# Performance work log

Hardware: AMD Instinct MI355X
Metric: run time of the kernel (lower is better)

Reference implementation:

```python
import jax, jax.numpy as jnp
import numpy as np
from functools import partial

C = 10   # number of regular-repr fields
G = 4    # C4 rotation group order
EPS = 1e-5


def _lift_kernel(w):
    """Lifting (trivial->regular) P4 kernel. w: [C, Cin, k, k] ->
    full kernel [C*G, Cin, k, k] with output channel layout (field, orientation)."""
    ks = [jnp.rot90(w, r, axes=(-2, -1)) for r in range(G)]  # each [C,Cin,k,k]
    k = jnp.stack(ks, axis=1)                                 # [C,G,Cin,k,k]
    return k.reshape(w.shape[0] * G, w.shape[1], w.shape[2], w.shape[3])


def _gconv_kernel(w):
    """Regular->regular P4 kernel. w: [Cout, Cin, G, k, k] (indexed by relative
    input orientation) -> full kernel [Cout*G, Cin*G, k, k].
    K[co*G+r, ci*G+s] = rot90(w[co, ci, (s-r) mod G], r)."""
    Cout, Cin, _, k1, k2 = w.shape
    ks = []
    for r in range(G):
        wr = jnp.roll(w, shift=r, axis=2)             # wr[..., s, :, :] = w[..., (s-r)%G]
        wr = jnp.rot90(wr, r, axes=(-2, -1))          # rotate spatially by r*90deg
        ks.append(wr)
    k = jnp.stack(ks, axis=1)                          # [Cout, G, Cin, G, k, k]
    return k.reshape(Cout * G, Cin * G, k1, k2)


def _conv(x, k, pad):
    return jax.lax.conv_general_dilated(
        x, k, window_strides=(1, 1), padding=pad,
        dimension_numbers=('NCHW', 'OIHW', 'NCHW'))


def _bn_relu(x, gamma, beta):
    """InnerBatchNorm (stats shared over the G orientations of each field) + ReLU."""
    B, CG, H, W = x.shape
    xr = x.reshape(B, C, G, H, W)
    m = xr.mean(axis=(0, 2, 3, 4), keepdims=True)
    v = xr.var(axis=(0, 2, 3, 4), keepdims=True)
    g = gamma[None, :, None, None, None]
    b = beta[None, :, None, None, None]
    y = (xr - m) * jax.lax.rsqrt(v + EPS) * g + b
    return jnp.maximum(y.reshape(B, CG, H, W), 0.0)


def _maxpool2(x):
    return jax.lax.reduce_window(x, -jnp.inf, jax.lax.max,
                                 (1, 1, 2, 2), (1, 1, 2, 2), 'VALID')


def setup_inputs() -> dict:
    key = jax.random.key(0)
    ks = jax.random.split(key, 20)
    B = 1024
    x = jax.random.normal(ks[0], (B, 1, 28, 28), dtype=jnp.float32)
    w1 = jax.random.normal(ks[1], (C, 1, 3, 3), dtype=jnp.float32) * 0.3
    w2 = jax.random.normal(ks[2], (C, C, G, 3, 3), dtype=jnp.float32) * 0.1
    w3 = jax.random.normal(ks[3], (C, C, G, 3, 3), dtype=jnp.float32) * 0.1
    w4 = jax.random.normal(ks[4], (C, C, G, 3, 3), dtype=jnp.float32) * 0.1
    w5 = jax.random.normal(ks[5], (C, C, G, 3, 3), dtype=jnp.float32) * 0.1
    w6 = jax.random.normal(ks[6], (C, C, G, 3, 3), dtype=jnp.float32) * 0.1
    w7 = jax.random.normal(ks[7], (C, C, G, 4, 4), dtype=jnp.float32) * 0.1
    g1 = jnp.ones((C,), jnp.float32) + 0.1 * jax.random.normal(ks[8], (C,))
    b1 = 0.1 * jax.random.normal(ks[9], (C,))
    g2 = jnp.ones((C,), jnp.float32) + 0.1 * jax.random.normal(ks[10], (C,))
    b2 = 0.1 * jax.random.normal(ks[11], (C,))
    gs = jnp.ones((C,), jnp.float32) + 0.1 * jax.random.normal(ks[12], (C,))
    bs = 0.1 * jax.random.normal(ks[13], (C,))
    wfc = jax.random.normal(ks[14], (10, C * 11 * 11), dtype=jnp.float32) * 0.05
    bfc = jnp.zeros((10,), jnp.float32)
    return dict(x=x, w1=w1, w2=w2, w3=w3, w4=w4, w5=w5, w6=w6, w7=w7,
                g1=g1, b1=b1, g2=g2, b2=b2, gs=gs, bs=bs, wfc=wfc, bfc=bfc)


PAD1 = [(1, 1), (1, 1)]
PAD0 = [(0, 0), (0, 0)]


def reference(x, w1, w2, w3, w4, w5, w6, w7, g1, b1, g2, b2, gs, bs, wfc, bfc):
    # block1: lifting P4 conv 3x3 pad1 + InnerBN + ReLU  -> [B, 40, 28, 28]
    h = _bn_relu(_conv(x, _lift_kernel(w1), PAD1), g1, b1)
    # block2: P4 conv + BN + ReLU + 2x2 max pool         -> [B, 40, 14, 14]
    h = _maxpool2(_bn_relu(_conv(h, _gconv_kernel(w2), PAD1), g2, b2))
    # blocks 3-6: P4 conv + shared BN/ReLU               -> [B, 40, 14, 14]
    for w in (w3, w4, w5, w6):
        h = _bn_relu(_conv(h, _gconv_kernel(w), PAD1), gs, bs)
    # block7: P4 conv 4x4 pad0 + shared BN/ReLU          -> [B, 40, 11, 11]
    h = _bn_relu(_conv(h, _gconv_kernel(w7), PAD0), gs, bs)
    # group pooling: max over the G orientations of each field -> [B, 10, 11, 11]
    B = h.shape[0]
    h = h.reshape(B, C, G, 11, 11).max(axis=2)
    # fc
    return h.reshape(B, -1) @ wfc.T + bfc
```

## Files before the change

kernel.cpp:

```cpp
#include <hip/hip_runtime.h>

#define EPSV 1e-5f
#define INV28 (1.f / 3211264.f)
#define INV14 (1.f / 802816.f)
#define INV11 (1.f / 495616.f)
#define NCOPY 64
#define LSTRIDE 2048

typedef _Float16 v8h __attribute__((ext_vector_type(8)));
typedef _Float16 v4h __attribute__((ext_vector_type(4)));
typedef _Float16 v2h __attribute__((ext_vector_type(2)));
typedef float v4f __attribute__((ext_vector_type(4)));

__device__ __forceinline__ int h2i(v2h v) { union { v2h h; int i; } u; u.h = v; return u.i; }
__device__ __forceinline__ v2h i2h(int i) { union { v2h h; int i; } u; u.i = i; return u.h; }
__device__ __forceinline__ int pmax2(int a, int b) {
  v2h x = i2h(a), y = i2h(b), r;
  r[0] = x[0] > y[0] ? x[0] : y[0];
  r[1] = x[1] > y[1] ? x[1] : y[1];
  return h2i(r);
}

__device__ __forceinline__ int rotsrc(int r, int dy, int dx, int K) {
  int sy, sx;
  if (r == 0)      { sy = dy;       sx = dx; }
  else if (r == 1) { sy = dx;       sx = K - 1 - dy; }
  else if (r == 2) { sy = K - 1 - dy; sx = K - 1 - dx; }
  else             { sy = K - 1 - dx; sx = dy; }
  return sy * K + sx;
}

__device__ __forceinline__ float gw_val(const float* __restrict__ w, int oc, int g,
                                        int j, int KS) {
  int tap = g / 5, cig = g % 5, ci = cig * 8 + j;
  int co = oc >> 2, r = oc & 3, cin = ci >> 2, s = ci & 3;
  int srel = (s - r) & 3;
  return w[((co * 10 + cin) * 4 + srel) * (KS * KS) + rotsrc(r, tap / KS, tap % KS, KS)];
}

__device__ __forceinline__ float statN(const float* __restrict__ p, int i) {
  float v = 0.f;
#pragma unroll
  for (int c = 0; c < NCOPY; ++c) v += p[c * 32 + i];
  return v;
}

__global__ void prep_kernel(const float* __restrict__ w1, const float* __restrict__ w2,
                            const float* __restrict__ w3, const float* __restrict__ w4,
                            const float* __restrict__ w5, const float* __restrict__ w6,
                            const float* __restrict__ w7,
                            _Float16* __restrict__ K1h, _Float16* __restrict__ Wh,
                            float* __restrict__ stats) {
  int idx = blockIdx.x * blockDim.x + threadIdx.x;
  if (idx < 7 * LSTRIDE) { stats[idx] = 0.f; return; }
  idx -= 7 * LSTRIDE;
  if (idx < 1536) {
    int mt = idx >> 9, l = (idx >> 3) & 63, j = idx & 7;
    int m = l & 15, quad = l >> 4;
    int k = quad * 8 + j, oc = mt * 16 + m;
    float val = 0.f;
    if (k < 9 && oc < 40) {
      int c = oc >> 2, r = oc & 3;
      val = w1[c * 9 + rotsrc(r, k / 3, k % 3, 3)];
    }
    K1h[idx] = (_Float16)val;
    return;
  }
  idx -= 1536;
  if (idx < 92160) {
    int l = idx / 18432, r0 = idx % 18432;
    const float* w = (l == 0) ? w2 : (l == 1) ? w3 : (l == 2) ? w4 : (l == 3) ? w5 : w6;
    int mt = r0 / 6144, r1 = r0 % 6144;
    int c = r1 / 512, r2 = r1 % 512;
    int q = r2 / 128, r3 = r2 % 128;
    int ocl = r3 / 8, j = r3 % 8;
    int oc = mt * 16 + ocl, g = c * 4 + q;
    float val = 0.f;
    if (oc < 40 && g < 45) val = gw_val(w, oc, g, j, 3);
    Wh[idx] = (_Float16)val;
    return;
  }
  idx -= 92160;
  if (idx < 30720) {
    int mt = idx / 10240, r1 = idx % 10240;
    int c = r1 / 512, r2 = r1 % 512;
    int q = r2 / 128, r3 = r2 % 128;
    int ocl = r3 / 8, j = r3 % 8;
    int oc = mt * 16 + ocl, g = c * 4 + q;
    float val = 0.f;
    if (oc < 40) val = gw_val(w7, oc, g, j, 4);
    Wh[92160 + idx] = (_Float16)val;
  }
}

__global__ __launch_bounds__(256) void conv1_stats(
    const float* __restrict__ x, const _Float16* __restrict__ K1h,
    float* __restrict__ stats) {
  __shared__ float ximg[900];
  __shared__ float sstat[20];
  const int tid = threadIdx.x, img = blockIdx.x;
  if (tid < 20) sstat[tid] = 0.f;
  for (int i = tid; i < 900; i += 256) {
    int gy = i / 30 - 1, gx = i % 30 - 1;
    ximg[i] = (gy >= 0 && gy < 28 && gx >= 0 && gx < 28)
                  ? x[img * 784 + gy * 28 + gx] : 0.f;
  }
  __syncthreads();
  const int lane = tid & 63, wv = tid >> 6;
  const int m = lane & 15, quad = lane >> 4;
  v8h a1[3];
#pragma unroll
  for (int mt = 0; mt < 3; ++mt)
    a1[mt] = *(const v8h*)(K1h + (mt * 64 + lane) * 8);
  float s[3] = {0.f, 0.f, 0.f}, q[3] = {0.f, 0.f, 0.f};
  for (int st = wv; st < 49; st += 4) {
    const int p = st * 16 + m;
    const int y = p / 28, xx = p % 28;
    v8h b;
#pragma unroll
    for (int j = 0; j < 8; ++j) {
      const int t = quad * 8 + j;
      float v = 0.f;
      if (t < 9) v = ximg[(y + t / 3) * 30 + xx + t % 3];
      b[j] = (_Float16)v;
    }
#pragma unroll
    for (int mt = 0; mt < 3; ++mt) {
      v4f acc = {0.f, 0.f, 0.f, 0.f};
      acc = __builtin_amdgcn_mfma_f32_16x16x32_f16(a1[mt], b, acc, 0, 0, 0);
#pragma unroll
      for (int r = 0; r < 4; ++r) { float v = acc[r]; s[mt] += v; q[mt] += v * v; }
    }
  }
#pragma unroll
  for (int mt = 0; mt < 3; ++mt) {
    float sv = s[mt], qv = q[mt];
#pragma unroll
    for (int off = 1; off <= 8; off <<= 1) {
      sv += __shfl_xor(sv, off, 64);
      qv += __shfl_xor(qv, off, 64);
    }
    if (m == 0 && ((mt < 2) || (quad < 2))) {
      atomicAdd(&sstat[mt * 4 + quad], sv);
      atomicAdd(&sstat[10 + mt * 4 + quad], qv);
    }
  }
  __syncthreads();
  if (tid < 20) atomicAdd(&stats[(blockIdx.x & (NCOPY - 1)) * 32 + tid], sstat[tid]);
}

template<int R>
__device__ __forceinline__ void band_impl(
    const int img, const int y0,
    const float* __restrict__ x, const _Float16* __restrict__ K1h,
    const _Float16* __restrict__ Wl,
    float* __restrict__ xpatch, _Float16* __restrict__ tile,
    const float* __restrict__ sc, const float* __restrict__ sh,
    float* __restrict__ sstat, _Float16* __restrict__ T0) {
  constexpr int NPIX = R * 28, NSUB = NPIX / 16, NSW = (NSUB + 3) / 4;
  constexpr int SROWS = R + 2, XR = R + 4;
  const int tid = threadIdx.x;
  const int lane = tid & 63, wv = tid >> 6;
  const int m = lane & 15, quad = lane >> 4;

  for (int i = tid; i < XR * 32; i += 256) {
    int gy = y0 - 2 + i / 32, gx = i % 32 - 2;
    xpatch[i] = (gy >= 0 && gy < 28 && gx >= 0 && gx < 28)
                    ? x[(long)img * 784 + gy * 28 + gx] : 0.f;
  }
  __syncthreads();

  {
    v8h a1[3];
#pragma unroll
    for (int mt = 0; mt < 3; ++mt)
      a1[mt] = *(const v8h*)(K1h + (mt * 64 + lane) * 8);
    constexpr int NPIXS = SROWS * 30;
    constexpr int NST = (NPIXS + 15) / 16;
    for (int st = wv; st < NST; st += 4) {
      const int p = st * 16 + m;
      const int pc = p < NPIXS ? p : NPIXS - 1;
      const int iy = pc / 30, ix = pc % 30;
      v8h b;
#pragma unroll
      for (int j = 0; j < 8; ++j) {
        const int t = quad * 8 + j;
        float v = 0.f;
        if (t < 9) v = xpatch[(iy + t / 3) * 32 + ix + t % 3];
        b[j] = (_Float16)v;
      }
      const int gy = y0 + iy - 1, gx = ix - 1;
      const bool wr = p < NPIXS;
      const bool inb = wr && gy >= 0 && gy < 28 && gx >= 0 && gx < 28;
      _Float16* tb = &tile[pc * 40];
#pragma unroll
      for (int mt = 0; mt < 3; ++mt) {
        v4f a = {0.f, 0.f, 0.f, 0.f};
        a = __builtin_amdgcn_mfma_f32_16x16x32_f16(a1[mt], b, a, 0, 0, 0);
        if (((mt < 2) || (quad < 2)) && wr) {
          const int f = mt * 4 + quad;
          const float scf = sc[f], shf = sh[f];
          v4h pk;
#pragma unroll
          for (int r = 0; r < 4; ++r)
            pk[r] = inb ? (_Float16)fmaxf(0.f, fmaf(a[r], scf, shf)) : (_Float16)0.f;
          *(v4h*)(tb + mt * 16 + quad * 4) = pk;
        }
      }
    }
  }
  __syncthreads();

  int pbase[NSW];
  bool sv[NSW];
#pragma unroll
  for (int s = 0; s < NSW; ++s) {
    int ns = wv + 4 * s;
    sv[s] = ns < NSUB;
    int i = (sv[s] ? ns : 0) * 16 + m;
    int q = i >> 2, c2 = i & 3;
    int yy = 2 * (q / 14) + (c2 >> 1), xx = 2 * (q % 14) + (c2 & 1);
    pbase[s] = (yy * 30 + xx) * 40;
  }
  v4f acc[3][NSW] = {};

  const _Float16* wlane = Wl + (quad * 16 + m) * 8;
  for (int c = 0; c < 12; ++c) {
    int g = 4 * c + quad; g = g > 44 ? 44 : g;
    int tap = g / 5, cig = g - tap * 5;
    int boff = ((tap / 3) * 30 + (tap % 3)) * 40 + cig * 8;
    v8h bfr[NSW];
#pragma unroll
    for (int s = 0; s < NSW; ++s)
      if (sv[s]) bfr[s] = *(const v8h*)&tile[pbase[s] + boff];
    v8h afr[3];
#pragma unroll
    for (int mt = 0; mt < 3; ++mt)
      afr[mt] = *(const v8h*)(wlane + (mt * 12 + c) * 512);
#pragma unroll
    for (int s = 0; s < NSW; ++s)
      if (sv[s]) {
#pragma unroll
        for (int mt = 0; mt < 3; ++mt)
          acc[mt][s] = __builtin_amdgcn_mfma_f32_16x16x32_f16(afr[mt], bfr[s],
                                                             acc[mt][s], 0, 0, 0);
      }
  }

#pragma unroll
  for (int mt = 0; mt < 3; ++mt) {
    float svv = 0.f, qvv = 0.f;
#pragma unroll
    for (int s = 0; s < NSW; ++s)
      if (sv[s]) {
#pragma unroll
        for (int r = 0; r < 4; ++r) { float v = acc[mt][s][r]; svv += v; qvv += v * v; }
      }
    const bool ocok = (mt < 2) || (quad < 2);
#pragma unroll
    for (int off = 1; off <= 8; off <<= 1) {
      svv += __shfl_xor(svv, off, 64);
      qvv += __shfl_xor(qvv, off, 64);
    }
    if (m == 0 && ocok) {
      atomicAdd(&sstat[mt * 4 + quad], svv);
      atomicAdd(&sstat[10 + mt * 4 + quad], qvv);
    }
  }

#pragma unroll
  for (int s = 0; s < NSW; ++s) {
    if (!sv[s]) continue;
    const int ns = wv + 4 * s;
    const int q = ns * 4 + (m >> 2);
    const int tb4 = (img * 256 + (y0 / 2 + q / 14 + 1) * 16 + (q % 14 + 1)) * 40;
#pragma unroll
    for (int mt = 0; mt < 3; ++mt) {
      const bool ocok = (mt < 2) || (quad < 2);
      if (!ocok) continue;
      v2h w0, w1;
      w0[0] = (_Float16)acc[mt][s][0]; w0[1] = (_Float16)acc[mt][s][1];
      w1[0] = (_Float16)acc[mt][s][2]; w1[1] = (_Float16)acc[mt][s][3];
      int a0 = h2i(w0), a1 = h2i(w1);
      a0 = pmax2(a0, __shfl_xor(a0, 1, 64));
      a0 = pmax2(a0, __shfl_xor(a0, 2, 64));
      a1 = pmax2(a1, __shfl_xor(a1, 1, 64));
      a1 = pmax2(a1, __shfl_xor(a1, 2, 64));
      if ((m & 3) == 0) {
        v2h r0 = i2h(a0), r1 = i2h(a1);
        v4h o;
        o[0] = r0[0]; o[1] = r0[1]; o[2] = r1[0]; o[3] = r1[1];
        *(v4h*)(T0 + (long)tb4 + mt * 16 + quad * 4) = o;
      }
    }
  }
}

__global__ __launch_bounds__(256) void conv_band_all(
    const float* __restrict__ x, const _Float16* __restrict__ K1h,
    const _Float16* __restrict__ Wl, const float* __restrict__ pstats,
    const float* __restrict__ pgamma, const float* __restrict__ pbeta,
    _Float16* __restrict__ T0, float* __restrict__ stats) {
  __shared__ __attribute__((aligned(16))) _Float16 tile[6 * 30 * 40];
  __shared__ float xpatch[8 * 32];
  __shared__ float sc[10], sh[10], sstat[20];
  const int tid = threadIdx.x;
  if (tid < 20) sstat[tid] = 0.f;
  if (tid >= 32 && tid < 42) {
    int f = tid - 32;
    float mu = statN(pstats, f) * INV28, q = statN(pstats, 10 + f) * INV28;
    float isd = rsqrtf(q - mu * mu + EPSV);
    float s = pgamma[f] * isd;
    sc[f] = s; sh[f] = pbeta[f] - mu * s;
  }
  const int bid = blockIdx.x;
  const int img = bid / 7, y0 = (bid % 7) * 4;
  band_impl<4>(img, y0, x, K1h, Wl, xpatch, tile, sc, sh, sstat, T0);
  __syncthreads();
  if (tid < 20) atomicAdd(&stats[(bid & (NCOPY - 1)) * 32 + tid], sstat[tid]);
}

__global__ __launch_bounds__(256) void conv_tile(
    _Float16* T, const _Float16* __restrict__ Wl,
    const float* __restrict__ pstats, const float* __restrict__ pg,
    const float* __restrict__ pb, float pinvn, float* __restrict__ stG) {
  __shared__ __attribute__((aligned(16))) _Float16 tile[256 * 40];
  __shared__ v2h scH[10], shH[10];
  __shared__ float sstat[20];
  const int tid = threadIdx.x, img = blockIdx.x;
  const int lane = tid & 63, wv = tid >> 6;
  const int m = lane & 15, quad = lane >> 4;
  if (tid < 20) sstat[tid] = 0.f;
  if (tid >= 32 && tid < 42) {
    int f = tid - 32;
    float mu = statN(pstats, f) * pinvn, q = statN(pstats, 10 + f) * pinvn;
    float isd = rsqrtf(q - mu * mu + EPSV);
    float s = pg[f] * isd;
    _Float16 sH = (_Float16)s, hH = (_Float16)(pb[f] - mu * s);
    v2h t0, t1;
    t0[0] = sH; t0[1] = sH; t1[0] = hH; t1[1] = hH;
    scH[f] = t0; shH[f] = t1;
  }
  __syncthreads();
  {
    const int iy = tid >> 4, ix = tid & 15;
    const bool border = (iy == 0) | (iy == 15) | (ix == 0) | (ix == 15);
    const _Float16* src = T + ((long)img * 256 + tid) * 40;
    _Float16* dst = &tile[tid * 40];
    if (!border) {
#pragma unroll
      for (int cg5 = 0; cg5 < 5; ++cg5) {
        v8h rv = *(const v8h*)(src + cg5 * 8);
        v2h* r2 = (v2h*)&rv;
        v8h pk; v2h* p2 = (v2h*)&pk;
#pragma unroll
        for (int pr = 0; pr < 4; ++pr) {
          const int f = cg5 * 2 + (pr >> 1);
          v2h t = r2[pr] * scH[f] + shH[f];
          v2h o;
          o[0] = t[0] > (_Float16)0.f ? t[0] : (_Float16)0.f;
          o[1] = t[1] > (_Float16)0.f ? t[1] : (_Float16)0.f;
          p2[pr] = o;
        }
        *(v8h*)(dst + cg5 * 8) = pk;
      }
    } else {
      v8h z;
#pragma unroll
      for (int u = 0; u < 8; ++u) z[u] = (_Float16)0.f;
#pragma unroll
      for (int cg5 = 0; cg5 < 5; ++cg5) *(v8h*)(dst + cg5 * 8) = z;
    }
  }
  __syncthreads();

  int pb3[4], n3[4];
  bool sv3[4], va3[4];
#pragma unroll
  for (int s = 0; s < 4; ++s) {
    int ns = wv + 4 * s;
    sv3[s] = ns < 13;
    int n = ns * 16 + m;
    va3[s] = sv3[s] && (n < 196);
    n = n < 196 ? n : 195;
    n3[s] = n;
    pb3[s] = ((n / 14) * 16 + (n % 14)) * 40;
  }
  const int wofs = (quad * 16 + m) * 8;
  v4f acc[3][4];
#pragma unroll
  for (int mt = 0; mt < 3; ++mt)
#pragma unroll
    for (int s = 0; s < 4; ++s) acc[mt][s] = (v4f){0.f, 0.f, 0.f, 0.f};
  for (int c = 0; c < 12; ++c) {
    int g = 4 * c + quad; g = g > 44 ? 44 : g;
    int tap = g / 5, cig = g - tap * 5;
    int boff = ((tap / 3) * 16 + (tap % 3)) * 40 + cig * 8;
    v8h bfr[4];
#pragma unroll
    for (int s = 0; s < 4; ++s)
      if (sv3[s]) bfr[s] = *(const v8h*)&tile[pb3[s] + boff];
    v8h afr[3];
#pragma unroll
    for (int mt = 0; mt < 3; ++mt)
      afr[mt] = *(const v8h*)(Wl + wofs + (mt * 12 + c) * 512);
#pragma unroll
    for (int s = 0; s < 4; ++s)
      if (sv3[s]) {
#pragma unroll
        for (int mt = 0; mt < 3; ++mt)
          acc[mt][s] = __builtin_amdgcn_mfma_f32_16x16x32_f16(afr[mt], bfr[s],
                                                             acc[mt][s], 0, 0, 0);
      }
  }

#pragma unroll
  for (int mt = 0; mt < 3; ++mt) {
    float svv = 0.f, qvv = 0.f;
#pragma unroll
    for (int s = 0; s < 4; ++s)
      if (va3[s]) {
#pragma unroll
        for (int r = 0; r < 4; ++r) { float v = acc[mt][s][r]; svv += v; qvv += v * v; }
      }
    const bool ocok = (mt < 2) || (quad < 2);
#pragma unroll
    for (int off = 1; off <= 8; off <<= 1) {
      svv += __shfl_xor(svv, off, 64);
      qvv += __shfl_xor(qvv, off, 64);
    }
    if (m == 0 && ocok) {
      atomicAdd(&sstat[mt * 4 + quad], svv);
      atomicAdd(&sstat[10 + mt * 4 + quad], qvv);
    }
  }
  __syncthreads();
  if (tid < 20) atomicAdd(&stG[(blockIdx.x & (NCOPY - 1)) * 32 + tid], sstat[tid]);

#pragma unroll
  for (int mt = 0; mt < 3; ++mt) {
    const bool ocok = (mt < 2) || (quad < 2);
    if (!ocok) continue;
#pragma unroll
    for (int s = 0; s < 4; ++s)
      if (va3[s]) {
        v4h pk;
#pragma unroll
        for (int r = 0; r < 4; ++r) pk[r] = (_Float16)acc[mt][s][r];
        const int n = n3[s];
        *(v4h*)(T + ((long)img * 256 + (n / 14 + 1) * 16 + (n % 14 + 1)) * 40
                + mt * 16 + quad * 4) = pk;
      }
  }
}

__global__ __launch_bounds__(256) void conv7_tile(
    const _Float16* __restrict__ Tin, const _Float16* __restrict__ Wl,
    const float* __restrict__ pstats, const float* __restrict__ pg,
    const float* __restrict__ pb,
    _Float16* __restrict__ T7, float* __restrict__ stG) {
  __shared__ __attribute__((aligned(16))) _Float16 tile[256 * 40];
  __shared__ v2h scH[10], shH[10];
  __shared__ float sstat[20];
  const int tid = threadIdx.x, img = blockIdx.x;
  const int lane = tid & 63, wv = tid >> 6;
  const int m = lane & 15, quad = lane >> 4;
  if (tid < 20) sstat[tid] = 0.f;
  if (tid >= 32 && tid < 42) {
    int f = tid - 32;
    float mu = statN(pstats, f) * INV14, q = statN(pstats, 10 + f) * INV14;
    float isd = rsqrtf(q - mu * mu + EPSV);
    float s = pg[f] * isd;
    _Float16 sH = (_Float16)s, hH = (_Float16)(pb[f] - mu * s);
    v2h t0, t1;
    t0[0] = sH; t0[1] = sH; t1[0] = hH; t1[1] = hH;
    scH[f] = t0; shH[f] = t1;
  }
  __syncthreads();
  {
    const int iy = tid >> 4, ix = tid & 15;
    const bool border = (iy == 0) | (iy == 15) | (ix == 0) | (ix == 15);
    const _Float16* src = Tin + ((long)img * 256 + tid) * 40;
    _Float16* dst = &tile[tid * 40];
    if (!border) {
#pragma unroll
      for (int cg5 = 0; cg5 < 5; ++cg5) {
        v8h rv = *(const v8h*)(src + cg5 * 8);
        v2h* r2 = (v2h*)&rv;
        v8h pk; v2h* p2 = (v2h*)&pk;
#pragma unroll
        for (int pr = 0; pr < 4; ++pr) {
          const int f = cg5 * 2 + (pr >> 1);
          v2h t = r2[pr] * scH[f] + shH[f];
          v2h o;
          o[0] = t[0] > (_Float16)0.f ? t[0] : (_Float16)0.f;
          o[1] = t[1] > (_Float16)0.f ? t[1] : (_Float16)0.f;
          p2[pr] = o;
        }
        *(v8h*)(dst + cg5 * 8) = pk;
      }
    } else {
      v8h z;
#pragma unroll
      for (int u = 0; u < 8; ++u) z[u] = (_Float16)0.f;
#pragma unroll
      for (int cg5 = 0; cg5 < 5; ++cg5) *(v8h*)(dst + cg5 * 8) = z;
    }
  }
  __syncthreads();

  int pb7[2], n7[2];
  bool va7[2];
#pragma unroll
  for (int s = 0; s < 2; ++s) {
    int ns = wv + 4 * s;
    int n = ns * 16 + m;
    va7[s] = n < 121;
    n = n < 121 ? n : 120;
    n7[s] = n;
    pb7[s] = ((n / 11 + 1) * 16 + (n % 11 + 1)) * 40;
  }
  const int wofs = (quad * 16 + m) * 8;
  v4f acc[3][2];
#pragma unroll
  for (int mt = 0; mt < 3; ++mt)
#pragma unroll
    for (int s = 0; s < 2; ++s) acc[mt][s] = (v4f){0.f, 0.f, 0.f, 0.f};
  for (int c = 0; c < 20; ++c) {
    int g = 4 * c + quad;
    int tap = g / 5, cig = g - tap * 5;
    int boff = ((tap >> 2) * 16 + (tap & 3)) * 40 + cig * 8;
    v8h bfr[2];
#pragma unroll
    for (int s = 0; s < 2; ++s) bfr[s] = *(const v8h*)&tile[pb7[s] + boff];
    v8h afr[3];
#pragma unroll
    for (int mt = 0; mt < 3; ++mt)
      afr[mt] = *(const v8h*)(Wl + wofs + (mt * 20 + c) * 512);
#pragma unroll
    for (int s = 0; s < 2; ++s)
#pragma unroll
      for (int mt = 0; mt < 3; ++mt)
        acc[mt][s] = __builtin_amdgcn_mfma_f32_16x16x32_f16(afr[mt], bfr[s],
                                                           acc[mt][s], 0, 0, 0);
  }

#pragma unroll
  for (int mt = 0; mt < 3; ++mt) {
    float svv = 0.f, qvv = 0.f;
#pragma unroll
    for (int s = 0; s < 2; ++s)
      if (va7[s]) {
#pragma unroll
        for (int r = 0; r < 4; ++r) { float v = acc[mt][s][r]; svv += v; qvv += v * v; }
      }
    const bool ocok = (mt < 2) || (quad < 2);
#pragma unroll
    for (int off = 1; off <= 8; off <<= 1) {
      svv += __shfl_xor(svv, off, 64);
      qvv += __shfl_xor(qvv, off, 64);
    }
    if (m == 0 && ocok) {
      atomicAdd(&sstat[mt * 4 + quad], svv);
      atomicAdd(&sstat[10 + mt * 4 + quad], qvv);
    }
  }
  __syncthreads();
  if (tid < 20) atomicAdd(&stG[(blockIdx.x & (NCOPY - 1)) * 32 + tid], sstat[tid]);

#pragma unroll
  for (int mt = 0; mt < 3; ++mt) {
    const bool ocok = (mt < 2) || (quad < 2);
    if (!ocok) continue;
#pragma unroll
    for (int s = 0; s < 2; ++s)
      if (va7[s]) {
        v4h pk;
#pragma unroll
        for (int r = 0; r < 4; ++r) pk[r] = (_Float16)acc[mt][s][r];
        *(v4h*)(T7 + ((long)img * 121 + n7[s]) * 40 + mt * 16 + quad * 4) = pk;
      }
  }
}

__global__ __launch_bounds__(256) void head_kernel(
    const _Float16* __restrict__ T7, const float* __restrict__ stats7,
    const float* __restrict__ gs, const float* __restrict__ bs,
    const float* __restrict__ wfc, const float* __restrict__ bfc,
    float* __restrict__ out) {
  __shared__ float sc[10], sh[10];
  __shared__ float mbuf[1210];
  __shared__ float red[40];
  const int tid = threadIdx.x, img = blockIdx.x;
  if (tid < 10) {
    float mu = statN(stats7, tid) * INV11, q = statN(stats7, 10 + tid) * INV11;
    float isd = rsqrtf(q - mu * mu + EPSV);
    float s = gs[tid] * isd;
    sc[tid] = s;
    sh[tid] = bs[tid] - mu * s;
  }
  __syncthreads();
  for (int p = tid; p < 121; p += 256) {
    const _Float16* rp = T7 + ((long)img * 121 + p) * 40;
#pragma unroll
    for (int cg5 = 0; cg5 < 5; ++cg5) {
      v8h v = *(const v8h*)(rp + cg5 * 8);
#pragma unroll
      for (int fh = 0; fh < 2; ++fh) {
        const int f = cg5 * 2 + fh;
        float mx = fmaf((float)v[fh * 4], sc[f], sh[f]);
#pragma unroll
        for (int r = 1; r < 4; ++r)
          mx = fmaxf(mx, fmaf((float)v[fh * 4 + r], sc[f], sh[f]));
        mbuf[f * 121 + p] = fmaxf(0.f, mx);
      }
    }
  }
  __syncthreads();
  const int wv = tid >> 6;
  for (int k = 0; k < 10; ++k) {
    float p = 0.f;
    for (int j = tid; j < 1210; j += 256) p = fmaf(mbuf[j], wfc[k * 1210 + j], p);
#pragma unroll
    for (int off = 32; off > 0; off >>= 1) p += __shfl_xor(p, off, 64);
    if ((tid & 63) == 0) red[k * 4 + wv] = p;
  }
  __syncthreads();
  if (tid < 10)
    out[img * 10 + tid] = bfc[tid] + red[tid * 4] + red[tid * 4 + 1] +
                          red[tid * 4 + 2] + red[tid * 4 + 3];
}

extern "C" void kernel_launch(void* const* d_in, const int* in_sizes, int n_in,
                              void* d_out, int out_size, void* d_ws, size_t ws_size,
                              hipStream_t stream) {
  const float* x   = (const float*)d_in[0];
  const float* w1  = (const float*)d_in[1];
  const float* w2  = (const float*)d_in[2];
  const float* w3  = (const float*)d_in[3];
  const float* w4  = (const float*)d_in[4];
  const float* w5  = (const float*)d_in[5];
  const float* w6  = (const float*)d_in[6];
  const float* w7  = (const float*)d_in[7];
  const float* g1  = (const float*)d_in[8];
  const float* b1  = (const float*)d_in[9];
  const float* g2  = (const float*)d_in[10];
  const float* b2  = (const float*)d_in[11];
  const float* gs  = (const float*)d_in[12];
  const float* bs  = (const float*)d_in[13];
  const float* wfc = (const float*)d_in[14];
  const float* bfc = (const float*)d_in[15];

  float* ws = (float*)d_ws;
  float* stats  = ws;
  _Float16* K1h = (_Float16*)(ws + 14336);
  _Float16* Wh  = (_Float16*)(ws + 15104);
  _Float16* T0  = (_Float16*)(ws + 76544);
  _Float16* T7  = (_Float16*)(ws + 5319424L);

  prep_kernel<<<543, 256, 0, stream>>>(w1, w2, w3, w4, w5, w6, w7, K1h, Wh, stats);
  conv1_stats<<<1024, 256, 0, stream>>>(x, K1h, stats);
  conv_band_all<<<7168, 256, 0, stream>>>(x, K1h, Wh, stats, g1, b1, T0,
                                          stats + LSTRIDE);
  conv_tile<<<1024, 256, 0, stream>>>(T0, Wh + 18432, stats + LSTRIDE, g2, b2, INV28,
                                      stats + 2 * LSTRIDE);
  conv_tile<<<1024, 256, 0, stream>>>(T0, Wh + 36864, stats + 2 * LSTRIDE, gs, bs, INV14,
                                      stats + 3 * LSTRIDE);
  conv_tile<<<1024, 256, 0, stream>>>(T0, Wh + 55296, stats + 3 * LSTRIDE, gs, bs, INV14,
                                      stats + 4 * LSTRIDE);
  conv_tile<<<1024, 256, 0, stream>>>(T0, Wh + 73728, stats + 4 * LSTRIDE, gs, bs, INV14,
                                      stats + 5 * LSTRIDE);
  conv7_tile<<<1024, 256, 0, stream>>>(T0, Wh + 92160, stats + 5 * LSTRIDE, gs, bs,
                                       T7, stats + 6 * LSTRIDE);
  head_kernel<<<1024, 256, 0, stream>>>(T7, stats + 6 * LSTRIDE, gs, bs, wfc, bfc,
                                        (float*)d_out);
}
```

Measured before the change: 311.6 us.

## Merge weight prep into conv1 stats kernel and shrink stat replica count

Folds the weight-packing prep kernel into the conv1 statistics kernel: the first 486 blocks pack the weights, and the remaining 1024 blocks compute per-image stats, building the lifting kernel fragments directly from w1 in registers. Stats zeroing moves to hipMemsetAsync. NCOPY drops from 64 to 8, so each stats read sums fewer replicas, at the cost of more atomic contention on each copy. This removes one kernel launch and the dependency between prep and conv1, but adds a memset node and redundant per-lane w1 gathers.

```diff
diff --git a/kernel.cpp b/kernel.cpp
--- a/kernel.cpp
+++ b/kernel.cpp
@@ -4,8 +4,8 @@
 #define INV28 (1.f / 3211264.f)
 #define INV14 (1.f / 802816.f)
 #define INV11 (1.f / 495616.f)
-#define NCOPY 64
-#define LSTRIDE 2048
+#define NCOPY 8
+#define LSTRIDE 256
 
 typedef _Float16 v8h __attribute__((ext_vector_type(8)));
 typedef _Float16 v4h __attribute__((ext_vector_type(4)));
@@ -38,6 +38,18 @@
   return w[((co * 10 + cin) * 4 + srel) * (KS * KS) + rotsrc(r, tap / KS, tap % KS, KS)];
 }
 
+__device__ __forceinline__ _Float16 k1_val(const float* __restrict__ w1,
+                                           int lane, int mt, int j) {
+  const int m = lane & 15, quad = lane >> 4;
+  const int k = quad * 8 + j, oc = mt * 16 + m;
+  float val = 0.f;
+  if (k < 9 && oc < 40) {
+    int c = oc >> 2, r = oc & 3;
+    val = w1[c * 9 + rotsrc(r, k / 3, k % 3, 3)];
+  }
+  return (_Float16)val;
+}
+
 __device__ __forceinline__ float statN(const float* __restrict__ p, int i) {
   float v = 0.f;
 #pragma unroll
@@ -45,60 +57,54 @@
   return v;
 }
 
-__global__ void prep_kernel(const float* __restrict__ w1, const float* __restrict__ w2,
-                            const float* __restrict__ w3, const float* __restrict__ w4,
-                            const float* __restrict__ w5, const float* __restrict__ w6,
-                            const float* __restrict__ w7,
-                            _Float16* __restrict__ K1h, _Float16* __restrict__ Wh,
-                            float* __restrict__ stats) {
-  int idx = blockIdx.x * blockDim.x + threadIdx.x;
-  if (idx < 7 * LSTRIDE) { stats[idx] = 0.f; return; }
-  idx -= 7 * LSTRIDE;
-  if (idx < 1536) {
-    int mt = idx >> 9, l = (idx >> 3) & 63, j = idx & 7;
-    int m = l & 15, quad = l >> 4;
-    int k = quad * 8 + j, oc = mt * 16 + m;
-    float val = 0.f;
-    if (k < 9 && oc < 40) {
-      int c = oc >> 2, r = oc & 3;
-      val = w1[c * 9 + rotsrc(r, k / 3, k % 3, 3)];
-    }
-    K1h[idx] = (_Float16)val;
-    return;
-  }
-  idx -= 1536;
-  if (idx < 92160) {
-    int l = idx / 18432, r0 = idx % 18432;
-    const float* w = (l == 0) ? w2 : (l == 1) ? w3 : (l == 2) ? w4 : (l == 3) ? w5 : w6;
-    int mt = r0 / 6144, r1 = r0 % 6144;
-    int c = r1 / 512, r2 = r1 % 512;
-    int q = r2 / 128, r3 = r2 % 128;
-    int ocl = r3 / 8, j = r3 % 8;
-    int oc = mt * 16 + ocl, g = c * 4 + q;
-    float val = 0.f;
-    if (oc < 40 && g < 45) val = gw_val(w, oc, g, j, 3);
-    Wh[idx] = (_Float16)val;
-    return;
-  }
-  idx -= 92160;
-  if (idx < 30720) {
-    int mt = idx / 10240, r1 = idx % 10240;
-    int c = r1 / 512, r2 = r1 % 512;
-    int q = r2 / 128, r3 = r2 % 128;
-    int ocl = r3 / 8, j = r3 % 8;
-    int oc = mt * 16 + ocl, g = c * 4 + q;
-    float val = 0.f;
-    if (oc < 40) val = gw_val(w7, oc, g, j, 4);
-    Wh[92160 + idx] = (_Float16)val;
-  }
-}
-
-__global__ __launch_bounds__(256) void conv1_stats(
-    const float* __restrict__ x, const _Float16* __restrict__ K1h,
+__global__ __launch_bounds__(256) void prep_stats(
+    const float* __restrict__ x,
+    const float* __restrict__ w1, const float* __restrict__ w2,
+    const float* __restrict__ w3, const float* __restrict__ w4,
+    const float* __restrict__ w5, const float* __restrict__ w6,
+    const float* __restrict__ w7,
+    _Float16* __restrict__ K1h, _Float16* __restrict__ Wh,
     float* __restrict__ stats) {
   __shared__ float ximg[900];
   __shared__ float sstat[20];
-  const int tid = threadIdx.x, img = blockIdx.x;
+  const int tid = threadIdx.x;
+  if (blockIdx.x < 486) {
+    int idx = blockIdx.x * blockDim.x + tid;
+    if (idx < 1536) {
+      int mt = idx >> 9, l = (idx >> 3) & 63, j = idx & 7;
+      K1h[idx] = k1_val(w1, l, mt, j);
+      return;
+    }
+    idx -= 1536;
+    if (idx < 92160) {
+      int l = idx / 18432, r0 = idx % 18432;
+      const float* w = (l == 0) ? w2 : (l == 1) ? w3 : (l == 2) ? w4
+                                                : (l == 3) ? w5 : w6;
+      int mt = r0 / 6144, r1 = r0 % 6144;
+      int c = r1 / 512, r2 = r1 % 512;
+      int q = r2 / 128, r3 = r2 % 128;
+      int ocl = r3 / 8, j = r3 % 8;
+      int oc = mt * 16 + ocl, g = c * 4 + q;
+      float val = 0.f;
+      if (oc < 40 && g < 45) val = gw_val(w, oc, g, j, 3);
+      Wh[idx] = (_Float16)val;
+      return;
+    }
+    idx -= 92160;
+    {
+      int mt = idx / 10240, r1 = idx % 10240;
+      int c = r1 / 512, r2 = r1 % 512;
+      int q = r2 / 128, r3 = r2 % 128;
+      int ocl = r3 / 8, j = r3 % 8;
+      int oc = mt * 16 + ocl, g = c * 4 + q;
+      float val = 0.f;
+      if (oc < 40) val = gw_val(w7, oc, g, j, 4);
+      Wh[92160 + idx] = (_Float16)val;
+    }
+    return;
+  }
+
+  const int img = blockIdx.x - 486;
   if (tid < 20) sstat[tid] = 0.f;
   for (int i = tid; i < 900; i += 256) {
     int gy = i / 30 - 1, gx = i % 30 - 1;
@@ -111,7 +117,8 @@
   v8h a1[3];
 #pragma unroll
   for (int mt = 0; mt < 3; ++mt)
-    a1[mt] = *(const v8h*)(K1h + (mt * 64 + lane) * 8);
+#pragma unroll
+    for (int j = 0; j < 8; ++j) a1[mt][j] = k1_val(w1, lane, mt, j);
   float s[3] = {0.f, 0.f, 0.f}, q[3] = {0.f, 0.f, 0.f};
   for (int st = wv; st < 49; st += 4) {
     const int p = st * 16 + m;
@@ -146,7 +153,7 @@
     }
   }
   __syncthreads();
-  if (tid < 20) atomicAdd(&stats[(blockIdx.x & (NCOPY - 1)) * 32 + tid], sstat[tid]);
+  if (tid < 20) atomicAdd(&stats[(img & (NCOPY - 1)) * 32 + tid], sstat[tid]);
 }
 
 template<int R>
@@ -653,13 +660,14 @@
 
   float* ws = (float*)d_ws;
   float* stats  = ws;
-  _Float16* K1h = (_Float16*)(ws + 14336);
-  _Float16* Wh  = (_Float16*)(ws + 15104);
-  _Float16* T0  = (_Float16*)(ws + 76544);
-  _Float16* T7  = (_Float16*)(ws + 5319424L);
-
-  prep_kernel<<<543, 256, 0, stream>>>(w1, w2, w3, w4, w5, w6, w7, K1h, Wh, stats);
-  conv1_stats<<<1024, 256, 0, stream>>>(x, K1h, stats);
+  _Float16* K1h = (_Float16*)(ws + 1792);
+  _Float16* Wh  = (_Float16*)(ws + 2560);
+  _Float16* T0  = (_Float16*)(ws + 64000);
+  _Float16* T7  = (_Float16*)(ws + 5306880L);
+
+  hipMemsetAsync(stats, 0, 7 * LSTRIDE * sizeof(float), stream);
+  prep_stats<<<1510, 256, 0, stream>>>(x, w1, w2, w3, w4, w5, w6, w7,
+                                       K1h, Wh, stats);
   conv_band_all<<<7168, 256, 0, stream>>>(x, K1h, Wh, stats, g1, b1, T0,
                                           stats + LSTRIDE);
   conv_tile<<<1024, 256, 0, stream>>>(T0, Wh + 18432, stats + LSTRIDE, g2, b2, INV28,
```

Result: faster. 270.3 us (-13.3%).
